# Optimization experiments

Hardware: AMD Instinct MI355X
Metric: run time of the kernel (lower is better)

## Reference

```python
import jax, jax.numpy as jnp
import numpy as np

H = 96
W = 96
FX = 96.0
FY = 96.0
NEAR = 0.3
EPS = 1e-8


def q2r(quat):
    # quat: [N,4] (w,x,y,z) -> [N,3,3]
    q = quat / (jnp.linalg.norm(quat, axis=-1, keepdims=True) + 1e-12)
    w, x, y, z = q[:, 0], q[:, 1], q[:, 2], q[:, 3]
    R = jnp.stack([
        1 - 2 * (y * y + z * z), 2 * (x * y - w * z), 2 * (x * z + w * y),
        2 * (x * y + w * z), 1 - 2 * (x * x + z * z), 2 * (y * z - w * x),
        2 * (x * z - w * y), 2 * (y * z + w * x), 1 - 2 * (x * x + y * y),
    ], axis=-1).reshape(-1, 3, 3)
    return R


def setup_inputs() -> dict:
    key = jax.random.key(0)
    ks = jax.random.split(key, 8)
    N = 4096
    pos_xy = jax.random.uniform(ks[0], (N, 2), minval=-2.0, maxval=2.0, dtype=jnp.float32)
    pos_z = jax.random.uniform(ks[1], (N, 1), minval=2.0, maxval=6.0, dtype=jnp.float32)
    pos = jnp.concatenate([pos_xy, pos_z], axis=-1)
    rgb = jax.random.normal(ks[2], (N, 3), dtype=jnp.float32)
    opa = jax.random.normal(ks[3], (N,), dtype=jnp.float32)
    quat = jax.random.normal(ks[4], (N, 4), dtype=jnp.float32)
    scale = jax.random.uniform(ks[5], (N, 3), dtype=jnp.float32) * 0.05 + 0.005
    rot = jnp.eye(3, dtype=jnp.float32)
    tran = jnp.zeros(3, dtype=jnp.float32)
    return {"pos": pos, "rgb": rgb, "opa": opa, "quat": quat, "scale": scale, "rot": rot, "tran": tran}


def reference(pos, rgb, opa, quat, scale, rot, tran):
    # ---- project: world -> camera -> image space ----
    cam = pos @ rot.T + tran[None, :]              # [N,3]
    x, y, z = cam[:, 0], cam[:, 1], cam[:, 2]
    r = jnp.linalg.norm(cam, axis=-1)              # depth = ray length (camera_to_image)
    mean2d = jnp.stack([x / z, y / z], axis=-1)    # [N,2]

    # jacobian of (x/z, y/z, |p|) wrt camera-space point, [N,3,3]
    zeros = jnp.zeros_like(z)
    J = jnp.stack([
        1.0 / z, zeros, -x / (z * z),
        zeros, 1.0 / z, -y / (z * z),
        x / r, y / r, z / r,
    ], axis=-1).reshape(-1, 3, 3)

    # ---- 3D covariance: R S S^T R^T ----
    R = q2r(quat)                                   # [N,3,3]
    s = jnp.abs(scale) + 1e-4                       # [N,3]
    RS = R * s[:, None, :]                          # R @ diag(s)
    cov3d = jnp.einsum('nij,nkj->nik', RS, RS)      # [N,3,3]

    # ---- 2D covariance: (J W) cov3d (J W)^T, upper-left 2x2 ----
    JW = jnp.einsum('nij,jk->nik', J, rot)          # [N,3,3]
    cov2d = jnp.einsum('nij,njk,nlk->nil', JW, cov3d, JW)[:, :2, :2]  # [N,2,2]

    a = cov2d[:, 0, 0] + EPS
    d = cov2d[:, 1, 1] + EPS
    b = 0.5 * (cov2d[:, 0, 1] + cov2d[:, 1, 0])
    det = a * d - b * b
    inv_a = d / det
    inv_b = -b / det
    inv_d = a / det

    rgb_act = jax.nn.sigmoid(rgb)                   # [N,3]
    opa_act = jax.nn.sigmoid(opa)                   # [N]

    # ---- per-pixel gaussian evaluation in normalized image space ----
    u = (jnp.arange(W, dtype=jnp.float32) + 0.5 - W / 2) / FX   # [W]
    v = (jnp.arange(H, dtype=jnp.float32) + 0.5 - H / 2) / FY   # [H]
    pu = jnp.tile(u, H)                                          # [P]
    pv = jnp.repeat(v, W)                                        # [P]

    dx = pu[None, :] - mean2d[:, 0:1]               # [N,P]
    dy = pv[None, :] - mean2d[:, 1:2]               # [N,P]
    power = -0.5 * (inv_a[:, None] * dx * dx + 2.0 * inv_b[:, None] * dx * dy + inv_d[:, None] * dy * dy)
    alpha = opa_act[:, None] * jnp.exp(power)       # [N,P]
    alpha = jnp.clip(alpha, 0.0, 0.99)
    valid = (z > NEAR).astype(alpha.dtype)[:, None]
    alpha = alpha * valid

    # ---- depth-sorted alpha compositing ----
    order = jnp.argsort(r)                          # near -> far
    alpha_s = alpha[order]                          # [N,P]
    rgb_s = rgb_act[order]                          # [N,3]

    log_1m = jnp.log1p(-alpha_s)                    # [N,P]
    cum = jnp.cumsum(log_1m, axis=0)
    logT = jnp.concatenate([jnp.zeros((1, alpha_s.shape[1]), alpha_s.dtype), cum[:-1]], axis=0)
    w = jnp.exp(logT) * alpha_s                     # [N,P] blending weights
    img = jnp.einsum('np,nc->pc', w, rgb_s)         # [P,3]
    return img.reshape(H, W, 3)
```

## Files before the change

kernel.cpp:

```cpp
#include <hip/hip_runtime.h>
#include <math.h>

#define N_G   4096
#define IMW   96
#define TILE  6
#define TILES_X 16
#define NTILE (TILES_X*TILES_X)
#define NTHR  1024
#define NW    (NTHR/64)
#define NST   (N_G/NTHR)
#define NPX   (TILE*TILE)
#define NSEG  16
#define BCAP  2048
#define CAP   512
#define FXI   (1.0f/96.0f)
#define NEARP 0.3f
#define EPSV  1e-8f
#define LOG2E 1.4426950408889634f
#define LN2   0.6931471805599453f
#define CULL_K 26.0f

typedef unsigned long long ull;
typedef __attribute__((ext_vector_type(2))) unsigned long long ull2;

__global__ __launch_bounds__(NTHR, 1) void splat_k(
    const float* __restrict__ pos, const float* __restrict__ rgb,
    const float* __restrict__ opa, const float* __restrict__ quat,
    const float* __restrict__ scale, const float* __restrict__ rot,
    const float* __restrict__ tran, float* __restrict__ out)
{
    __shared__ unsigned int bl[BCAP];
    __shared__ __align__(16) ull skey[CAP+2];
    __shared__ int sslot[CAP];
    __shared__ float4 g0[CAP], g1[CAP];
    __shared__ float  g2[CAP];
    __shared__ float4 pix[NSEG*NPX];
    __shared__ int psum[2][CAP];
    __shared__ int bcnt_sh, cnt_sh;

    const int t = threadIdx.x;
    const int tile = blockIdx.x;
    const int tx = tile % TILES_X, ty = tile / TILES_X;
    const float u0 = ((float)(tx*TILE) + 0.5f - 48.0f) * FXI;
    const float u1 = u0 + (TILE-1) * FXI;
    const float v0 = ((float)(ty*TILE) + 0.5f - 48.0f) * FXI;
    const float v1 = v0 + (TILE-1) * FXI;
    const int lane = t & 63;

    if (t == 0) { bcnt_sh = 0; cnt_sh = 0; }

    float R00=rot[0],R01=rot[1],R02=rot[2];
    float R10=rot[3],R11=rot[4],R12=rot[5];
    float R20=rot[6],R21=rot[7],R22=rot[8];
    float t0=tran[0], t1=tran[1], t2=tran[2];

    float pp0[NST], pp1[NST], pp2[NST], po[NST], ps0[NST], ps1[NST], ps2[NST];
    #pragma unroll
    for (int st = 0; st < NST; st++) {
        int gi = st*NTHR + t;
        pp0[st]=pos[gi*3+0]; pp1[st]=pos[gi*3+1]; pp2[st]=pos[gi*3+2];
        po[st]=opa[gi];
        ps0[st]=scale[gi*3+0]; ps1[st]=scale[gi*3+1]; ps2[st]=scale[gi*3+2];
    }
    __syncthreads();

    #pragma unroll
    for (int st = 0; st < NST; st++) {
        int gi = st*NTHR + t;
        float x = R00*pp0[st] + R01*pp1[st] + R02*pp2[st] + t0;
        float y = R10*pp0[st] + R11*pp1[st] + R12*pp2[st] + t1;
        float z = R20*pp0[st] + R21*pp1[st] + R22*pp2[st] + t2;
        float invz = 1.0f/z;
        float mu = x*invz, mv = y*invz;

        float inz2 = invz*invz;
        float fn = 2.0f*inz2 + (x*x + y*y)*inz2*inz2;
        float smax = fmaxf(fmaxf(fabsf(ps0[st]), fabsf(ps1[st])), fabsf(ps2[st])) + 1e-4f;
        float lmax = fn*smax*smax + EPSV;
        float amp = CULL_K + 1.0f + fminf(0.0f, po[st]*LOG2E);
        float r2b = amp * lmax * (2.0f*LN2) * 1.02f;

        float cu = fminf(fmaxf(mu, u0), u1);
        float cv = fminf(fmaxf(mv, v0), v1);
        float ddx = mu - cu, ddy = mv - cv;
        bool flag = (z > NEARP) && (amp > 0.0f) && (ddx*ddx + ddy*ddy <= r2b);

        ull m = __ballot(flag);
        int nm = __popcll(m);
        int base = 0;
        if (lane == 0 && nm) base = atomicAdd(&bcnt_sh, nm);
        base = __shfl(base, 0);
        if (flag) {
            int p = base + __popcll(m & ((1ull << lane) - 1ull));
            if (p < BCAP) bl[p] = (unsigned int)gi;
        }
    }
    __syncthreads();
    int bcnt = bcnt_sh; if (bcnt > BCAP) bcnt = BCAP;

    for (int s0i = 0; s0i < bcnt; s0i += NTHR) {
        int s = s0i + t;
        bool flag = false;
        float4 o0, o1; float ocb = 0.0f, rr = 0.0f;
        unsigned int gi = 0;
        if (s < bcnt) {
            gi = bl[s];
            float p0=pos[gi*3+0], p1=pos[gi*3+1], p2=pos[gi*3+2];
            float x = R00*p0 + R01*p1 + R02*p2 + t0;
            float y = R10*p0 + R11*p1 + R12*p2 + t1;
            float z = R20*p0 + R21*p1 + R22*p2 + t2;
            rr = sqrtf(x*x + y*y + z*z);
            float invz = 1.0f/z;
            float mu = x*invz, mv = y*invz;

            float J02 = -x*invz*invz, J12 = -y*invz*invz;
            float JW00 = invz*R00 + J02*R20;
            float JW01 = invz*R01 + J02*R21;
            float JW02 = invz*R02 + J02*R22;
            float JW10 = invz*R10 + J12*R20;
            float JW11 = invz*R11 + J12*R21;
            float JW12 = invz*R12 + J12*R22;

            float qw=quat[gi*4+0], qx=quat[gi*4+1], qy=quat[gi*4+2], qz=quat[gi*4+3];
            float qn = sqrtf(qw*qw+qx*qx+qy*qy+qz*qz) + 1e-12f;
            float qi = 1.0f/qn;
            qw*=qi; qx*=qi; qy*=qi; qz*=qi;
            float Q00=1.f-2.f*(qy*qy+qz*qz), Q01=2.f*(qx*qy-qw*qz), Q02=2.f*(qx*qz+qw*qy);
            float Q10=2.f*(qx*qy+qw*qz), Q11=1.f-2.f*(qx*qx+qz*qz), Q12=2.f*(qy*qz-qw*qx);
            float Q20=2.f*(qx*qz-qw*qy), Q21=2.f*(qy*qz+qw*qx), Q22=1.f-2.f*(qx*qx+qy*qy);

            float sa=fabsf(scale[gi*3+0])+1e-4f;
            float sb=fabsf(scale[gi*3+1])+1e-4f;
            float sc=fabsf(scale[gi*3+2])+1e-4f;
            float A00=Q00*sa,A01=Q01*sb,A02=Q02*sc;
            float A10=Q10*sa,A11=Q11*sb,A12=Q12*sc;
            float A20=Q20*sa,A21=Q21*sb,A22=Q22*sc;
            float C00=A00*A00+A01*A01+A02*A02;
            float C01=A00*A10+A01*A11+A02*A12;
            float C02=A00*A20+A01*A21+A02*A22;
            float C11=A10*A10+A11*A11+A12*A12;
            float C12=A10*A20+A11*A21+A12*A22;
            float C22=A20*A20+A21*A21+A22*A22;
            float M00=JW00*C00+JW01*C01+JW02*C02;
            float M01=JW00*C01+JW01*C11+JW02*C12;
            float M02=JW00*C02+JW01*C12+JW02*C22;
            float M10=JW10*C00+JW11*C01+JW12*C02;
            float M11=JW10*C01+JW11*C11+JW12*C12;
            float M12=JW10*C02+JW11*C12+JW12*C22;
            float a  = M00*JW00+M01*JW01+M02*JW02 + EPSV;
            float d  = M10*JW10+M11*JW11+M12*JW12 + EPSV;
            float bb = 0.5f*((M00*JW10+M01*JW11+M02*JW12)+(M10*JW00+M11*JW01+M12*JW02));
            float invdet = 1.0f/(a*d - bb*bb);
            float iaP = -0.5f*d*invdet*LOG2E;
            float ibP =  bb*invdet*LOG2E;
            float idP = -0.5f*a*invdet*LOG2E;

            float sig_o = 1.0f/(1.0f+__expf(-opa[gi]));
            float opa_eff = (z > NEARP) ? sig_o : 0.0f;

            float q00 = -iaP, q01 = -0.5f*ibP, q11 = -idP;
            float df = q00 - q11;
            float lam = 0.5f*((q00 + q11) - sqrtf(df*df + 4.0f*q01*q01));
            lam = fmaxf(lam, 1e-20f);
            float r2 = (CULL_K + log2f(opa_eff)) / lam;

            float cu = fminf(fmaxf(mu, u0), u1);
            float cv = fminf(fmaxf(mv, v0), v1);
            float ddx = mu - cu, ddy = mv - cv;
            flag = (ddx*ddx + ddy*ddy) <= r2;

            if (flag) {
                float c0 = 1.0f/(1.0f+__expf(-rgb[gi*3+0]));
                float c1 = 1.0f/(1.0f+__expf(-rgb[gi*3+1]));
                float c2 = 1.0f/(1.0f+__expf(-rgb[gi*3+2]));
                o0 = make_float4(mu, mv, iaP, ibP);
                o1 = make_float4(idP, opa_eff, c0, c1);
                ocb = c2;
            }
        }
        ull m = __ballot(flag);
        int nm = __popcll(m);
        int base = 0;
        if (lane == 0 && nm) base = atomicAdd(&cnt_sh, nm);
        base = __shfl(base, 0);
        if (flag) {
            int p = base + __popcll(m & ((1ull << lane) - 1ull));
            if (p < CAP) {
                g0[p] = o0; g1[p] = o1; g2[p] = ocb;
                skey[p] = ((ull)__float_as_uint(rr) << 32) | gi;
            }
        }
    }
    __syncthreads();
    int cnt = cnt_sh; if (cnt > CAP) cnt = CAP;

    if (t == 0 && (cnt & 1)) skey[cnt] = ~0ull;
    __syncthreads();
    int cnt2 = cnt + (cnt & 1);
    int h = ((cnt2 >> 1) + 1) & ~1;
    if (h > cnt2) h = cnt2;
    const int g = t >> 9, e = t & 511;
    ull v = 0;
    if (e < cnt) {
        v = skey[e];
        const ull2* sk2 = (const ull2*)skey;
        int wA = g ? (h >> 1) : 0;
        int wB = g ? (cnt2 >> 1) : (h >> 1);
        int c = 0;
        for (int w = wA; w < wB; w++) {
            ull2 p = sk2[w];
            c += (p.x < v) ? 1 : 0;
            c += (p.y < v) ? 1 : 0;
        }
        psum[g][e] = c;
    }
    __syncthreads();
    if (t < cnt) {
        int r = psum[0][t] + psum[1][t];
        skey[r]  = v;
        sslot[r] = t;
    }
    __syncthreads();

    if (t < NSEG*NPX) {
        const int seg = t / NPX, pid = t % NPX;
        const int px = tx*TILE + (pid % TILE);
        const int py = ty*TILE + (pid / TILE);
        const float pu = ((float)px + 0.5f - 48.0f) * FXI;
        const float pv = ((float)py + 0.5f - 48.0f) * FXI;

        const int per = (cnt + NSEG - 1) / NSEG;
        const int sA = min(seg * per, cnt);
        const int sB = min(sA + per, cnt);

        float T = 1.0f, cr = 0.0f, cg = 0.0f, cb = 0.0f;
        for (int s = sA; s < sB; s++) {
            int slot = sslot[s];
            float4 a0 = g0[slot];
            float4 a1 = g1[slot];
            float  a2 = g2[slot];
            float dx = pu - a0.x;
            float dy = pv - a0.y;
            float pw = dx*(a0.z*dx + a0.w*dy) + a1.x*dy*dy;
            float al = fminf(a1.y * __builtin_amdgcn_exp2f(pw), 0.99f);
            float w = T * al;
            cr += w * a1.z;
            cg += w * a1.w;
            cb += w * a2;
            T *= (1.0f - al);
        }
        pix[t] = make_float4(cr, cg, cb, T);
    }
    __syncthreads();

    if (t < NPX) {
        float orr = 0.0f, og = 0.0f, ob = 0.0f, T2 = 1.0f;
        #pragma unroll
        for (int s = 0; s < NSEG; s++) {
            float4 P = pix[s*NPX + t];
            orr += T2 * P.x;
            og  += T2 * P.y;
            ob  += T2 * P.z;
            T2  *= P.w;
        }
        int px = tx*TILE + (t % TILE);
        int py = ty*TILE + (t / TILE);
        int pixel = py * IMW + px;
        out[pixel*3+0] = orr;
        out[pixel*3+1] = og;
        out[pixel*3+2] = ob;
    }
}

extern "C" void kernel_launch(void* const* d_in, const int* in_sizes, int n_in,
                              void* d_out, int out_size, void* d_ws, size_t ws_size,
                              hipStream_t stream) {
    const float* pos   = (const float*)d_in[0];
    const float* rgb   = (const float*)d_in[1];
    const float* opa   = (const float*)d_in[2];
    const float* quat  = (const float*)d_in[3];
    const float* scale = (const float*)d_in[4];
    const float* rot   = (const float*)d_in[5];
    const float* tran  = (const float*)d_in[6];
    float* out = (float*)d_out;

    splat_k<<<NTILE, NTHR, 0, stream>>>(pos, rgb, opa, quat, scale, rot, tran, out);
}
```

Baseline: 14.59 us.

## Split rank-sort across four groups for small counts; map segments to wavefronts

When at most 256 splats survive culling, the rank-counting sort splits the comparisons across four thread groups instead of two, which shortens each thread's serial loop. The compositing phase now gives each wavefront one segment, with lanes 0-35 as pixels, instead of packing 576 threads contiguously. Each wavefront then runs the loop over its own segment's range without divergence across segments, at the cost of idle lanes 36-63. The psum buffer doubles in size, and the sort takes a branch on the count.

```diff
diff --git a/kernel.cpp b/kernel.cpp
--- a/kernel.cpp
+++ b/kernel.cpp
@@ -35,7 +35,7 @@
     __shared__ float4 g0[CAP], g1[CAP];
     __shared__ float  g2[CAP];
     __shared__ float4 pix[NSEG*NPX];
-    __shared__ int psum[2][CAP];
+    __shared__ int psum[4][CAP];
     __shared__ int bcnt_sh, cnt_sh;
 
     const int t = threadIdx.x;
@@ -45,7 +45,7 @@
     const float u1 = u0 + (TILE-1) * FXI;
     const float v0 = ((float)(ty*TILE) + 0.5f - 48.0f) * FXI;
     const float v1 = v0 + (TILE-1) * FXI;
-    const int lane = t & 63;
+    const int wid = t >> 6, lane = t & 63;
 
     if (t == 0) { bcnt_sh = 0; cnt_sh = 0; }
 
@@ -197,33 +197,52 @@
     if (t == 0 && (cnt & 1)) skey[cnt] = ~0ull;
     __syncthreads();
     int cnt2 = cnt + (cnt & 1);
-    int h = ((cnt2 >> 1) + 1) & ~1;
-    if (h > cnt2) h = cnt2;
-    const int g = t >> 9, e = t & 511;
+    int nq = cnt2 >> 1;
+    const ull2* sk2 = (const ull2*)skey;
     ull v = 0;
-    if (e < cnt) {
-        v = skey[e];
-        const ull2* sk2 = (const ull2*)skey;
-        int wA = g ? (h >> 1) : 0;
-        int wB = g ? (cnt2 >> 1) : (h >> 1);
-        int c = 0;
-        for (int w = wA; w < wB; w++) {
-            ull2 p = sk2[w];
-            c += (p.x < v) ? 1 : 0;
-            c += (p.y < v) ? 1 : 0;
-        }
-        psum[g][e] = c;
+    bool small = (cnt <= 256);
+    if (small) {
+        const int g = t >> 8, e = t & 255;
+        if (e < cnt) {
+            v = skey[e];
+            int wA = (nq * g) >> 2;
+            int wB = (nq * (g+1)) >> 2;
+            int c = 0;
+            for (int w = wA; w < wB; w++) {
+                ull2 p = sk2[w];
+                c += (p.x < v) ? 1 : 0;
+                c += (p.y < v) ? 1 : 0;
+            }
+            psum[g][e] = c;
+        }
+    } else {
+        const int g = t >> 9, e = t & 511;
+        if (e < cnt) {
+            v = skey[e];
+            int wA = (nq * g) >> 1;
+            int wB = (nq * (g+1)) >> 1;
+            int c = 0;
+            for (int w = wA; w < wB; w++) {
+                ull2 p = sk2[w];
+                c += (p.x < v) ? 1 : 0;
+                c += (p.y < v) ? 1 : 0;
+            }
+            psum[g][e] = c;
+        }
     }
     __syncthreads();
     if (t < cnt) {
-        int r = psum[0][t] + psum[1][t];
+        int r = small ? (psum[0][t] + psum[1][t] + psum[2][t] + psum[3][t])
+                      : (psum[0][t] + psum[1][t]);
         skey[r]  = v;
         sslot[r] = t;
     }
     __syncthreads();
 
-    if (t < NSEG*NPX) {
-        const int seg = t / NPX, pid = t % NPX;
+    {
+        const int seg = wid;
+        const bool act = (lane < NPX);
+        const int pid = act ? lane : 0;
         const int px = tx*TILE + (pid % TILE);
         const int py = ty*TILE + (pid / TILE);
         const float pu = ((float)px + 0.5f - 48.0f) * FXI;
@@ -249,7 +268,7 @@
             cb += w * a2;
             T *= (1.0f - al);
         }
-        pix[t] = make_float4(cr, cg, cb, T);
+        if (act) pix[seg*NPX + pid] = make_float4(cr, cg, cb, T);
     }
     __syncthreads();
 
```

Result: faster. 14.22 us (-2.5%).
